# Performance work log

Hardware: AMD Instinct MI355X
Metric: run time of the kernel (lower is better)

The kernel has to match this reference:

```python
import jax, jax.numpy as jnp
import numpy as np


def setup_inputs() -> dict:
    key = jax.random.key(0)
    k1, k2 = jax.random.split(key)
    B, C, H, W = 8, 64, 128, 256
    src = jax.random.normal(k1, (B, C, H, W), dtype=jnp.float32)
    tgt = jax.random.normal(k2, (B, C, H, W), dtype=jnp.float32)
    return {"src": src, "tgt": tgt, "search_range": 4}


def reference(src, tgt, search_range):
    # Cost volume: for each (dy, dx) shift of tgt (zero-padded), channel dot with src.
    # Output channel ordering matches the torch loop: center, then for i=1..S:
    # (+i,0), (-i,0), (0,+i), (0,-i), then for j=1..S: (+i,+j), (-i,+j), (+i,-j), (-i,-j).
    S = search_range
    B, C, H, W = src.shape
    tgt_pad = jnp.pad(tgt, ((0, 0), (0, 0), (S, S), (S, S)))

    def cost(di, dj):
        # shifted[y, x] = tgt[y - di, x - dj] (zero outside)
        shifted = tgt_pad[:, :, S - di:S - di + H, S - dj:S - dj + W]
        return jnp.sum(shifted * src, axis=1)  # [B, H, W]

    outs = [cost(0, 0)]
    for i in range(1, S + 1):
        outs.extend([cost(i, 0), cost(-i, 0), cost(0, i), cost(0, -i)])
        for j in range(1, S + 1):
            outs.extend([cost(i, j), cost(-i, j), cost(i, -j), cost(-i, -j)])
    return jnp.stack(outs, axis=1)  # [B, (2S+1)^2, H, W]
```

## Files before the change

### kernel.cpp

```cpp
#include <hip/hip_runtime.h>

#define S    4
#define BB   8
#define CC   64
#define HH   128
#define WW   256
#define KCH  8
#define NCP  4
#define TH   4
#define TW   64
#define PX   4
#define NTX  16
#define TROWS 12
#define PITCHD 72
#define SPITCH 72
#define NT   576
#define NCH  (CC / KCH)
#define HW   (HH * WW)
#define TGTU (NCP * TROWS * 18)
#define SRCU (NCP * TH * 16)
#define L2SZ (NCP * TROWS * PITCHD)
#define LSSZ (NCP * TH * SPITCH)

typedef _Float16 h2 __attribute__((ext_vector_type(2)));

#if __has_builtin(__builtin_amdgcn_cvt_pkrtz)
__device__ inline h2 pack2(float x, float y) {
  return __builtin_bit_cast(h2, __builtin_amdgcn_cvt_pkrtz(x, y));
}
#else
__device__ inline h2 pack2(float x, float y) { h2 r; r[0] = (_Float16)x; r[1] = (_Float16)y; return r; }
#endif

#if __has_builtin(__builtin_amdgcn_fdot2)
__device__ inline float dot2(h2 a, h2 b, float c) { return __builtin_amdgcn_fdot2(a, b, c, false); }
#else
__device__ inline float dot2(h2 a, h2 b, float c) { return c + (float)a[0]*(float)b[0] + (float)a[1]*(float)b[1]; }
#endif

__device__ __host__ constexpr int ord_idx(int di, int dj) {
  int i = di < 0 ? -di : di;
  int j = dj < 0 ? -dj : dj;
  if (i == 0 && j == 0) return 0;
  if (j == 0) return 1 + (i - 1) * 20 + (di > 0 ? 0 : 1);
  if (i == 0) return 1 + (j - 1) * 20 + (dj > 0 ? 2 : 3);
  return 1 + (i - 1) * 20 + 4 + (j - 1) * 4 +
         (di > 0 ? (dj > 0 ? 0 : 2) : (dj > 0 ? 1 : 3));
}

__global__ __launch_bounds__(NT, 4)
void costvol_kernel(const float* __restrict__ src,
                    const float* __restrict__ tgt,
                    float* __restrict__ out) {
  __shared__ __align__(16) float lds2[2][L2SZ];
  __shared__ __align__(16) float ldss[2][LSSZ];

  const int tx  = threadIdx.x;
  const int ty  = threadIdx.y;
  const int tz  = threadIdx.z;
  const int tid = tz * 64 + ty * 16 + tx;
  const int bx  = blockIdx.x;
  const int by  = blockIdx.y;
  const int b   = blockIdx.z;

  const int w0b = bx * TW;
  const int h0  = by * TH;
  const int h   = h0 + ty;
  const int w0  = w0b + tx * PX;
  const int di  = tz - S;
  const int row = ty - tz + 8;

  int lofs0 = -1, goff0 = -1, lofs1 = -1, goff1 = -1;
#pragma unroll
  for (int k = 0; k < 2; ++k) {
    const int u = tid + k * NT;
    if (u < TGTU) {
      const int cp  = u / (TROWS * 18);
      const int rem = u - cp * (TROWS * 18);
      const int r   = rem / 18;
      const int wq  = rem - r * 18;
      const int gh  = h0 - S + r;
      const int gw  = w0b - S + 4 * wq;
      const int lo  = cp * (TROWS * PITCHD) + r * PITCHD + 4 * wq;
      int go = -1;
      if ((unsigned)gh < (unsigned)HH && gw >= 0 && gw + 3 < WW)
        go = ((b * CC + 2 * cp) * HW) + gh * WW + gw;
      if (k == 0) { lofs0 = lo; goff0 = go; } else { lofs1 = lo; goff1 = go; }
    }
  }

  const int scp = (tid >> 6) & 3;
  const int sr  = (tid >> 4) & 3;
  const int sq  = tid & 15;
  const int sgo = (b * CC + 2 * scp) * HW + (h0 + sr) * WW + w0b + 4 * sq;
  const int slo = (scp * TH + sr) * SPITCH + 4 * sq;

  float acc[9][PX];
#pragma unroll
  for (int o = 0; o < 9; ++o)
#pragma unroll
    for (int p = 0; p < PX; ++p) acc[o][p] = 0.f;

  float4 tA0, tB0, tA1, tB1, sA, sB;
  const float4 z4 = make_float4(0.f, 0.f, 0.f, 0.f);

#define ISSUE(CHN) do {                                                     \
    const int _off = (CHN) * (KCH * HW);                                    \
    tA0 = z4; tB0 = z4; tA1 = z4; tB1 = z4;                                 \
    if (goff0 >= 0) {                                                       \
      tA0 = *reinterpret_cast<const float4*>(tgt + goff0 + _off);           \
      tB0 = *reinterpret_cast<const float4*>(tgt + goff0 + _off + HW);      \
    }                                                                       \
    if (goff1 >= 0) {                                                       \
      tA1 = *reinterpret_cast<const float4*>(tgt + goff1 + _off);           \
      tB1 = *reinterpret_cast<const float4*>(tgt + goff1 + _off + HW);      \
    }                                                                       \
    if (tid < SRCU) {                                                       \
      sA = *reinterpret_cast<const float4*>(src + sgo + _off);              \
      sB = *reinterpret_cast<const float4*>(src + sgo + _off + HW);         \
    }                                                                       \
  } while (0)

#define PACKQ(VA, VB, DST) do {                                             \
    float4 _wv;                                                             \
    _wv.x = __builtin_bit_cast(float, pack2((VA).x, (VB).x));               \
    _wv.y = __builtin_bit_cast(float, pack2((VA).y, (VB).y));               \
    _wv.z = __builtin_bit_cast(float, pack2((VA).z, (VB).z));               \
    _wv.w = __builtin_bit_cast(float, pack2((VA).w, (VB).w));               \
    *reinterpret_cast<float4*>(DST) = _wv;                                  \
  } while (0)

  ISSUE(0);

  int s = 0;
  for (int ch = 0; ch < NCH; ++ch) {
    float* lb2w = &lds2[0][0] + s * L2SZ;
    float* lbsw = &ldss[0][0] + s * LSSZ;
    if (lofs0 >= 0) PACKQ(tA0, tB0, lb2w + lofs0);
    if (lofs1 >= 0) PACKQ(tA1, tB1, lb2w + lofs1);
    if (tid < SRCU) PACKQ(sA, sB, lbsw + slo);

    if (ch + 1 < NCH) ISSUE(ch + 1);

    __syncthreads();

    const float* lb2 = &lds2[0][0] + s * L2SZ;
    const float* lbs = &ldss[0][0] + s * LSSZ;
#pragma unroll
    for (int cp = 0; cp < NCP; ++cp) {
      const float4 st = *reinterpret_cast<const float4*>(
          lbs + (cp * TH + ty) * SPITCH + 4 * tx);
      const h2 sv[PX] = {__builtin_bit_cast(h2, st.x), __builtin_bit_cast(h2, st.y),
                         __builtin_bit_cast(h2, st.z), __builtin_bit_cast(h2, st.w)};

      const float* lp = lb2 + cp * (TROWS * PITCHD) + row * PITCHD + 4 * tx;
      h2 win[12];
#pragma unroll
      for (int q = 0; q < 3; ++q) {
        const float4 t = *reinterpret_cast<const float4*>(lp + 4 * q);
        win[4 * q]     = __builtin_bit_cast(h2, t.x);
        win[4 * q + 1] = __builtin_bit_cast(h2, t.y);
        win[4 * q + 2] = __builtin_bit_cast(h2, t.z);
        win[4 * q + 3] = __builtin_bit_cast(h2, t.w);
      }

#pragma unroll
      for (int dj = -S; dj <= S; ++dj) {
#pragma unroll
        for (int p = 0; p < PX; ++p)
          acc[dj + S][p] = dot2(sv[p], win[p - dj + 4], acc[dj + S][p]);
      }
    }

    s ^= 1;
  }

  const size_t HWs = (size_t)HW;
  float* op = out + (size_t)b * 81 * HWs + (size_t)h * WW + w0;
#pragma unroll
  for (int dj = -S; dj <= S; ++dj) {
    const int o    = ord_idx(di, dj);
    const int slot = dj + S;
    *reinterpret_cast<float4*>(op + (size_t)o * HWs) =
        make_float4(acc[slot][0], acc[slot][1], acc[slot][2], acc[slot][3]);
  }
}

extern "C" void kernel_launch(void* const* d_in, const int* in_sizes, int n_in,
                              void* d_out, int out_size, void* d_ws, size_t ws_size,
                              hipStream_t stream) {
  const float* src = (const float*)d_in[0];
  const float* tgt = (const float*)d_in[1];
  float* out = (float*)d_out;
  dim3 grid(WW / TW, HH / TH, BB);
  dim3 block(NTX, TH, 9);
  costvol_kernel<<<grid, block, 0, stream>>>(src, tgt, out);
}
```

Measured before the change: 67.78 us.

## Halve channel chunk and prefetch two chunks ahead with per-thread load roles

Cuts the channel chunk per stage from 8 to 4 and keeps two chunks of global loads in flight, issuing chunk n+2 while chunk n is written to LDS and computed. Load work is split so each thread loads either one tgt quad or one src quad instead of up to three, which lowers register pressure and balances loads across threads. The price is twice as many barriers per channel and less compute per stage to hide latency behind.

```diff
diff --git a/kernel.cpp b/kernel.cpp
--- a/kernel.cpp
+++ b/kernel.cpp
@@ -5,8 +5,8 @@
 #define CC   64
 #define HH   128
 #define WW   256
-#define KCH  8
-#define NCP  4
+#define KCH  4
+#define NCP  2
 #define TH   4
 #define TW   64
 #define PX   4
@@ -18,25 +18,18 @@
 #define NCH  (CC / KCH)
 #define HW   (HH * WW)
 #define TGTU (NCP * TROWS * 18)
-#define SRCU (NCP * TH * 16)
+#define SRCB 432
 #define L2SZ (NCP * TROWS * PITCHD)
 #define LSSZ (NCP * TH * SPITCH)
 
 typedef _Float16 h2 __attribute__((ext_vector_type(2)));
 
-#if __has_builtin(__builtin_amdgcn_cvt_pkrtz)
 __device__ inline h2 pack2(float x, float y) {
   return __builtin_bit_cast(h2, __builtin_amdgcn_cvt_pkrtz(x, y));
 }
-#else
-__device__ inline h2 pack2(float x, float y) { h2 r; r[0] = (_Float16)x; r[1] = (_Float16)y; return r; }
-#endif
-
-#if __has_builtin(__builtin_amdgcn_fdot2)
-__device__ inline float dot2(h2 a, h2 b, float c) { return __builtin_amdgcn_fdot2(a, b, c, false); }
-#else
-__device__ inline float dot2(h2 a, h2 b, float c) { return c + (float)a[0]*(float)b[0] + (float)a[1]*(float)b[1]; }
-#endif
+__device__ inline float dot2(h2 a, h2 b, float c) {
+  return __builtin_amdgcn_fdot2(a, b, c, false);
+}
 
 __device__ __host__ constexpr int ord_idx(int di, int dj) {
   int i = di < 0 ? -di : di;
@@ -70,30 +63,28 @@
   const int di  = tz - S;
   const int row = ty - tz + 8;
 
-  int lofs0 = -1, goff0 = -1, lofs1 = -1, goff1 = -1;
-#pragma unroll
-  for (int k = 0; k < 2; ++k) {
-    const int u = tid + k * NT;
-    if (u < TGTU) {
-      const int cp  = u / (TROWS * 18);
-      const int rem = u - cp * (TROWS * 18);
-      const int r   = rem / 18;
-      const int wq  = rem - r * 18;
-      const int gh  = h0 - S + r;
-      const int gw  = w0b - S + 4 * wq;
-      const int lo  = cp * (TROWS * PITCHD) + r * PITCHD + 4 * wq;
-      int go = -1;
-      if ((unsigned)gh < (unsigned)HH && gw >= 0 && gw + 3 < WW)
-        go = ((b * CC + 2 * cp) * HW) + gh * WW + gw;
-      if (k == 0) { lofs0 = lo; goff0 = go; } else { lofs1 = lo; goff1 = go; }
-    }
+  const bool tgtr = tid < TGTU;
+  const bool srcr = tid >= SRCB && tid < SRCB + 128;
+
+  int lofs = 0, goff = -1;
+  if (tgtr) {
+    const int cp  = tid / (TROWS * 18);
+    const int rem = tid - cp * (TROWS * 18);
+    const int r   = rem / 18;
+    const int wq  = rem - r * 18;
+    const int gh  = h0 - S + r;
+    const int gw  = w0b - S + 4 * wq;
+    lofs = cp * (TROWS * PITCHD) + r * PITCHD + 4 * wq;
+    if ((unsigned)gh < (unsigned)HH && gw >= 0 && gw + 3 < WW)
+      goff = ((b * CC + 2 * cp) * HW) + gh * WW + gw;
+  } else if (srcr) {
+    const int u   = tid - SRCB;
+    const int scp = u >> 6;
+    const int sr  = (u >> 4) & 3;
+    const int sq  = u & 15;
+    lofs = (scp * TH + sr) * SPITCH + 4 * sq;
+    goff = (b * CC + 2 * scp) * HW + (h0 + sr) * WW + w0b + 4 * sq;
   }
-
-  const int scp = (tid >> 6) & 3;
-  const int sr  = (tid >> 4) & 3;
-  const int sq  = tid & 15;
-  const int sgo = (b * CC + 2 * scp) * HW + (h0 + sr) * WW + w0b + 4 * sq;
-  const int slo = (scp * TH + sr) * SPITCH + 4 * sq;
 
   float acc[9][PX];
 #pragma unroll
@@ -101,78 +92,79 @@
 #pragma unroll
     for (int p = 0; p < PX; ++p) acc[o][p] = 0.f;
 
-  float4 tA0, tB0, tA1, tB1, sA, sB;
   const float4 z4 = make_float4(0.f, 0.f, 0.f, 0.f);
+  float4 fA0, fB0, fA1, fB1;
 
-#define ISSUE(CHN) do {                                                     \
+#define ISSUE(CHN, FA, FB) do {                                             \
     const int _off = (CHN) * (KCH * HW);                                    \
-    tA0 = z4; tB0 = z4; tA1 = z4; tB1 = z4;                                 \
-    if (goff0 >= 0) {                                                       \
-      tA0 = *reinterpret_cast<const float4*>(tgt + goff0 + _off);           \
-      tB0 = *reinterpret_cast<const float4*>(tgt + goff0 + _off + HW);      \
-    }                                                                       \
-    if (goff1 >= 0) {                                                       \
-      tA1 = *reinterpret_cast<const float4*>(tgt + goff1 + _off);           \
-      tB1 = *reinterpret_cast<const float4*>(tgt + goff1 + _off + HW);      \
-    }                                                                       \
-    if (tid < SRCU) {                                                       \
-      sA = *reinterpret_cast<const float4*>(src + sgo + _off);              \
-      sB = *reinterpret_cast<const float4*>(src + sgo + _off + HW);         \
+    if (tgtr) {                                                             \
+      FA = z4; FB = z4;                                                     \
+      if (goff >= 0) {                                                      \
+        FA = *reinterpret_cast<const float4*>(tgt + goff + _off);           \
+        FB = *reinterpret_cast<const float4*>(tgt + goff + _off + HW);      \
+      }                                                                     \
+    } else if (srcr) {                                                      \
+      FA = *reinterpret_cast<const float4*>(src + goff + _off);             \
+      FB = *reinterpret_cast<const float4*>(src + goff + _off + HW);        \
     }                                                                       \
   } while (0)
 
-#define PACKQ(VA, VB, DST) do {                                             \
-    float4 _wv;                                                             \
-    _wv.x = __builtin_bit_cast(float, pack2((VA).x, (VB).x));               \
-    _wv.y = __builtin_bit_cast(float, pack2((VA).y, (VB).y));               \
-    _wv.z = __builtin_bit_cast(float, pack2((VA).z, (VB).z));               \
-    _wv.w = __builtin_bit_cast(float, pack2((VA).w, (VB).w));               \
-    *reinterpret_cast<float4*>(DST) = _wv;                                  \
+#define WRITE(FA, FB, BUF) do {                                             \
+    if (tgtr | srcr) {                                                      \
+      float* _d = (tgtr ? &lds2[BUF][0] : &ldss[BUF][0]) + lofs;            \
+      float4 _wv;                                                           \
+      _wv.x = __builtin_bit_cast(float, pack2((FA).x, (FB).x));             \
+      _wv.y = __builtin_bit_cast(float, pack2((FA).y, (FB).y));             \
+      _wv.z = __builtin_bit_cast(float, pack2((FA).z, (FB).z));             \
+      _wv.w = __builtin_bit_cast(float, pack2((FA).w, (FB).w));             \
+      *reinterpret_cast<float4*>(_d) = _wv;                                 \
+    }                                                                       \
   } while (0)
 
-  ISSUE(0);
+#define COMPUTE(BUF) do {                                                   \
+    const float* lb2 = &lds2[BUF][0];                                       \
+    const float* lbs = &ldss[BUF][0];                                       \
+    _Pragma("unroll")                                                       \
+    for (int cp = 0; cp < NCP; ++cp) {                                      \
+      const float4 st = *reinterpret_cast<const float4*>(                   \
+          lbs + (cp * TH + ty) * SPITCH + 4 * tx);                          \
+      const h2 sv[PX] = {__builtin_bit_cast(h2, st.x),                      \
+                         __builtin_bit_cast(h2, st.y),                      \
+                         __builtin_bit_cast(h2, st.z),                      \
+                         __builtin_bit_cast(h2, st.w)};                     \
+      const float* lp = lb2 + cp * (TROWS * PITCHD) + row * PITCHD + 4*tx;  \
+      h2 win[12];                                                           \
+      _Pragma("unroll")                                                     \
+      for (int q = 0; q < 3; ++q) {                                         \
+        const float4 t = *reinterpret_cast<const float4*>(lp + 4 * q);      \
+        win[4 * q]     = __builtin_bit_cast(h2, t.x);                       \
+        win[4 * q + 1] = __builtin_bit_cast(h2, t.y);                       \
+        win[4 * q + 2] = __builtin_bit_cast(h2, t.z);                       \
+        win[4 * q + 3] = __builtin_bit_cast(h2, t.w);                       \
+      }                                                                     \
+      _Pragma("unroll")                                                     \
+      for (int dj = -S; dj <= S; ++dj) {                                    \
+        _Pragma("unroll")                                                   \
+        for (int p = 0; p < PX; ++p)                                        \
+          acc[dj + S][p] = dot2(sv[p], win[p - dj + 4], acc[dj + S][p]);    \
+      }                                                                     \
+    }                                                                       \
+  } while (0)
 
-  int s = 0;
-  for (int ch = 0; ch < NCH; ++ch) {
-    float* lb2w = &lds2[0][0] + s * L2SZ;
-    float* lbsw = &ldss[0][0] + s * LSSZ;
-    if (lofs0 >= 0) PACKQ(tA0, tB0, lb2w + lofs0);
-    if (lofs1 >= 0) PACKQ(tA1, tB1, lb2w + lofs1);
-    if (tid < SRCU) PACKQ(sA, sB, lbsw + slo);
+#define STEP(CHN, FA, FB, BUF) do {                                         \
+    WRITE(FA, FB, BUF);                                                     \
+    if ((CHN) + 2 < NCH) ISSUE((CHN) + 2, FA, FB);                          \
+    __syncthreads();                                                        \
+    COMPUTE(BUF);                                                           \
+  } while (0)
 
-    if (ch + 1 < NCH) ISSUE(ch + 1);
+  ISSUE(0, fA0, fB0);
+  ISSUE(1, fA1, fB1);
 
-    __syncthreads();
-
-    const float* lb2 = &lds2[0][0] + s * L2SZ;
-    const float* lbs = &ldss[0][0] + s * LSSZ;
-#pragma unroll
-    for (int cp = 0; cp < NCP; ++cp) {
-      const float4 st = *reinterpret_cast<const float4*>(
-          lbs + (cp * TH + ty) * SPITCH + 4 * tx);
-      const h2 sv[PX] = {__builtin_bit_cast(h2, st.x), __builtin_bit_cast(h2, st.y),
-                         __builtin_bit_cast(h2, st.z), __builtin_bit_cast(h2, st.w)};
-
-      const float* lp = lb2 + cp * (TROWS * PITCHD) + row * PITCHD + 4 * tx;
-      h2 win[12];
-#pragma unroll
-      for (int q = 0; q < 3; ++q) {
-        const float4 t = *reinterpret_cast<const float4*>(lp + 4 * q);
-        win[4 * q]     = __builtin_bit_cast(h2, t.x);
-        win[4 * q + 1] = __builtin_bit_cast(h2, t.y);
-        win[4 * q + 2] = __builtin_bit_cast(h2, t.z);
-        win[4 * q + 3] = __builtin_bit_cast(h2, t.w);
-      }
-
-#pragma unroll
-      for (int dj = -S; dj <= S; ++dj) {
-#pragma unroll
-        for (int p = 0; p < PX; ++p)
-          acc[dj + S][p] = dot2(sv[p], win[p - dj + 4], acc[dj + S][p]);
-      }
-    }
-
-    s ^= 1;
+#pragma unroll 1
+  for (int c2 = 0; c2 < NCH / 2; ++c2) {
+    STEP(2 * c2,     fA0, fB0, 0);
+    STEP(2 * c2 + 1, fA1, fB1, 1);
   }
 
   const size_t HWs = (size_t)HW;
```

Result: slower. 72.69 us (+7.2%).
